# Kernel tuning notes

Hardware: AMD Instinct MI355X
Metric: run time of the kernel (lower is better)

The kernel has to match this reference:

```python
import jax, jax.numpy as jnp
import numpy as np

N = 50000          # nodes
E = 800000         # edges (before self-loops)
IN_CH = 16
HID = 32
HEADS = 4
NEG_SLOPE = 0.2    # PyG GATConv default leaky_relu slope


def add_self_loops(edge_index, n):
    loops = jnp.arange(n, dtype=edge_index.dtype)
    return jnp.concatenate([edge_index, jnp.stack([loops, loops])], axis=1)


def gat_layer(x, edge_index, W, a_src, a_dst, bias, heads, out_ch, concat):
    """PyG-style GATConv: gather -> attention logits -> segment softmax over dst -> scatter."""
    n = x.shape[0]
    h = (x @ W).reshape(n, heads, out_ch)            # [N, H, C]
    src, dst = edge_index[0], edge_index[1]          # messages flow src -> dst
    alpha_src = (h * a_src).sum(-1)                  # [N, H]
    alpha_dst = (h * a_dst).sum(-1)                  # [N, H]
    e = jax.nn.leaky_relu(alpha_src[src] + alpha_dst[dst], NEG_SLOPE)  # [Etot, H]
    # numerically stable segment softmax over incoming edges of each dst node
    e_max = jax.ops.segment_max(e, dst, num_segments=n)
    e_exp = jnp.exp(e - e_max[dst])
    denom = jax.ops.segment_sum(e_exp, dst, num_segments=n)
    alpha = e_exp / (denom[dst] + 1e-16)             # [Etot, H]
    out = jax.ops.segment_sum(h[src] * alpha[..., None], dst, num_segments=n)  # [N, H, C]
    out = out.reshape(n, heads * out_ch) if concat else out.mean(axis=1)
    return out + bias


def setup_inputs() -> dict:
    key = jax.random.key(0)
    ks = jax.random.split(key, 10)
    x = jax.random.normal(ks[0], (N, IN_CH), dtype=jnp.float32)
    edge_index = jax.random.randint(ks[1], (2, E), 0, N, dtype=jnp.int64)
    s = 0.1
    W1 = jax.random.normal(ks[2], (IN_CH, HEADS * HID), dtype=jnp.float32) * s
    a_src1 = jax.random.normal(ks[3], (1, HEADS, HID), dtype=jnp.float32) * s
    a_dst1 = jax.random.normal(ks[4], (1, HEADS, HID), dtype=jnp.float32) * s
    b1 = jnp.zeros((HEADS * HID,), dtype=jnp.float32)
    W2 = jax.random.normal(ks[5], (HEADS * HID, 2), dtype=jnp.float32) * s
    a_src2 = jax.random.normal(ks[6], (1, 1, 2), dtype=jnp.float32) * s
    a_dst2 = jax.random.normal(ks[7], (1, 1, 2), dtype=jnp.float32) * s
    b2 = jnp.zeros((2,), dtype=jnp.float32)
    return {"x": x, "edge_index": edge_index,
            "W1": W1, "a_src1": a_src1, "a_dst1": a_dst1, "b1": b1,
            "W2": W2, "a_src2": a_src2, "a_dst2": a_dst2, "b2": b2}


def reference(x, edge_index, W1, a_src1, a_dst1, b1, W2, a_src2, a_dst2, b2):
    ei = add_self_loops(edge_index, x.shape[0])
    h = gat_layer(x, ei, W1, a_src1, a_dst1, b1, HEADS, HID, concat=True)
    h = jax.nn.relu(h)
    out = gat_layer(h, ei, W2, a_src2, a_dst2, b2, 1, 2, concat=False)
    return out
```

## Files before the change

kernel.cpp:

```cpp
#include <hip/hip_runtime.h>
#include <hip/hip_bf16.h>

#define N_NODES 50000
#define N_EDGES 800000
#define ETOT    (N_EDGES + N_NODES)
#define STRIDE  64
#define IN_CH   16
#define HID     32
#define HEADS   4
#define C1      (HEADS * HID)
#define NEG     0.2f

#define DEG_BLOCKS ((ETOT / 4 + 255) / 256)
#define NGROUPS    (N_NODES / 4)
#define H1_BLOCKS  2048

typedef unsigned short u16;
typedef unsigned int   u32;

__device__ __forceinline__ float bf2f(u16 b) {
    return __uint_as_float(((u32)b) << 16);
}

__device__ __forceinline__ u16 f2bf(float f) {
    __hip_bfloat16 hb = __float2bfloat16(f);
    return *(u16*)&hb;
}

__device__ __forceinline__ int clampn(int v) {
    return v < 0 ? 0 : (v >= N_NODES ? N_NODES - 1 : v);
}

__device__ __forceinline__ int eidx(const int* ei, int e, int i64, int which) {
    int v = i64 ? ei[2 * (which * N_EDGES + e)] : ei[which * N_EDGES + e];
    return clampn(v);
}

__device__ __forceinline__ float cvt(const void* src, int i, int bf) {
    return bf ? bf2f(((const u16*)src)[i]) : ((const float*)src)[i];
}

__device__ __forceinline__ int probe_bf_wave(const u16* xb) {
    int l = threadIdx.x & 63;
    int my = 0;
#pragma unroll
    for (int k = 0; k < 4; k++) {
        float f = bf2f(xb[l * 4 + k]);
        float a = fabsf(f);
        if (f == 0.0f || (a > 9.5e-7f && a < 1.05e6f)) my++;
    }
#pragma unroll
    for (int m = 32; m; m >>= 1) my += __shfl_xor(my, m);
    return my >= 224;
}

__device__ __forceinline__ int probe_i64_wave(const int* ei32) {
    int l = threadIdx.x & 63;
    int nz = (l < 32 && ei32[2 * l + 1] != 0) ? 1 : 0;
#pragma unroll
    for (int m = 32; m; m >>= 1) nz += __shfl_xor(nz, m);
    return nz == 0;
}

__device__ __forceinline__ void dev_deg(const int* __restrict__ ei,
                                        int* __restrict__ degs,
                                        u32* __restrict__ srp, int blk) {
    int i64 = probe_i64_wave(ei);
    int e0 = (blk * 256 + (int)threadIdx.x) * 4;
    if (e0 >= ETOT) return;
    int s[4], d[4];
#pragma unroll
    for (int j = 0; j < 4; j++) {
        int e = e0 + j;
        if (e < N_EDGES) { s[j] = eidx(ei, e, i64, 0); d[j] = eidx(ei, e, i64, 1); }
        else             { s[j] = d[j] = e - N_EDGES; }
    }
    u32 r[4];
#pragma unroll
    for (int j = 0; j < 4; j++) {
        u32 rr = (u32)atomicAdd(&degs[d[j]], 1);
        r[j] = ((u32)s[j] << 16) | (rr > 0xFFFFu ? 0xFFFFu : rr);
    }
    *(uint4*)(srp + e0) = make_uint4(r[0], r[1], r[2], r[3]);
}

__device__ __forceinline__ void dev_fill(const int* __restrict__ ei,
                                         const u32* __restrict__ srp,
                                         u16* __restrict__ csr, int blk) {
    int i64 = probe_i64_wave(ei);
    int e0 = (blk * 256 + (int)threadIdx.x) * 4;
    if (e0 >= ETOT) return;
    uint4 q = *(const uint4*)(srp + e0);
    u32 sr[4] = {q.x, q.y, q.z, q.w};
#pragma unroll
    for (int j = 0; j < 4; j++) {
        int e = e0 + j;
        int d = (e < N_EDGES) ? eidx(ei, e, i64, 1) : (e - N_EDGES);
        u32 r = sr[j] & 0xFFFFu;
        if (r < STRIDE) csr[d * STRIDE + r] = (u16)(sr[j] >> 16);
    }
}

__device__ __forceinline__ void dev_h1(const void* __restrict__ x,
                                       const void* __restrict__ W1,
                                       const void* __restrict__ a_s,
                                       const void* __restrict__ a_d,
                                       u32* __restrict__ h1u,
                                       float* __restrict__ as1,
                                       float* __restrict__ ad1,
                                       float* Ws, float* As, float* Ad, int blk) {
    int bf = probe_bf_wave((const u16*)x);
    if (blk == 0 && threadIdx.x < 4) as1[N_NODES * 4 + threadIdx.x] = -1e30f;
    if (bf) {
        const u32* w32 = (const u32*)W1;
        for (int i = threadIdx.x; i < IN_CH * C1 / 2; i += 256) {
            u32 v = w32[i];
            Ws[2 * i]     = bf2f((u16)(v & 0xFFFF));
            Ws[2 * i + 1] = bf2f((u16)(v >> 16));
        }
        const u32* s32 = (const u32*)a_s;
        const u32* d32 = (const u32*)a_d;
        for (int i = threadIdx.x; i < C1 / 2; i += 256) {
            u32 vs = s32[i], vd = d32[i];
            As[2 * i]     = bf2f((u16)(vs & 0xFFFF));
            As[2 * i + 1] = bf2f((u16)(vs >> 16));
            Ad[2 * i]     = bf2f((u16)(vd & 0xFFFF));
            Ad[2 * i + 1] = bf2f((u16)(vd >> 16));
        }
    } else {
        for (int i = threadIdx.x; i < IN_CH * C1; i += 256) Ws[i] = ((const float*)W1)[i];
        for (int i = threadIdx.x; i < C1; i += 256) {
            As[i] = ((const float*)a_s)[i];
            Ad[i] = ((const float*)a_d)[i];
        }
    }
    __syncthreads();

    int w = threadIdx.x >> 6, l = threadIdx.x & 63;
    int c0 = 2 * l, c1 = 2 * l + 1;
    for (int g = blk; g < NGROUPS; g += H1_BLOCKS) {
        int n = g * 4 + w;
        float xval = (l < IN_CH) ? cvt(x, n * IN_CH + l, bf) : 0.f;
        float acc0 = 0.f, acc1 = 0.f;
#pragma unroll
        for (int k = 0; k < IN_CH; k++) {
            float xk = __shfl(xval, k);
            acc0 += xk * Ws[k * C1 + c0];
            acc1 += xk * Ws[k * C1 + c1];
        }
        h1u[n * 64 + l] = (u32)f2bf(acc0) | ((u32)f2bf(acc1) << 16);

        float ps = acc0 * As[c0] + acc1 * As[c1];
        float pd = acc0 * Ad[c0] + acc1 * Ad[c1];
#pragma unroll
        for (int m = 8; m; m >>= 1) { ps += __shfl_xor(ps, m); pd += __shfl_xor(pd, m); }
        if ((l & 15) == 0) {
            int hd = l >> 4;
            as1[n * 4 + hd] = ps;
            ad1[n * 4 + hd] = pd;
        }
    }
}

__launch_bounds__(256)
__global__ void k_deg(const int* __restrict__ ei, int* __restrict__ degs,
                      u32* __restrict__ srp) {
    dev_deg(ei, degs, srp, blockIdx.x);
}

__launch_bounds__(256)
__global__ void k_fill_h1(const void* __restrict__ x, const int* __restrict__ ei,
                          const void* __restrict__ W1, const void* __restrict__ a_s,
                          const void* __restrict__ a_d, const u32* __restrict__ srp,
                          u16* __restrict__ csr, u32* __restrict__ h1u,
                          float* __restrict__ as1, float* __restrict__ ad1) {
    __shared__ float Ws[IN_CH * C1];
    __shared__ float As[C1], Ad[C1];
    if (blockIdx.x < DEG_BLOCKS) { dev_fill(ei, srp, csr, blockIdx.x); return; }
    dev_h1(x, W1, a_s, a_d, h1u, as1, ad1, Ws, As, Ad, blockIdx.x - DEG_BLOCKS);
}

__launch_bounds__(256)
__global__ void k_fill(const int* __restrict__ ei, const u32* __restrict__ srp,
                       u16* __restrict__ csr) {
    dev_fill(ei, srp, csr, blockIdx.x);
}

__launch_bounds__(256)
__global__ void k_h1_only(const void* __restrict__ x, const void* __restrict__ W1,
                          const void* __restrict__ a_s, const void* __restrict__ a_d,
                          u32* __restrict__ h1u, float* __restrict__ as1,
                          float* __restrict__ ad1) {
    __shared__ float Ws[IN_CH * C1];
    __shared__ float As[C1], Ad[C1];
    dev_h1(x, W1, a_s, a_d, h1u, as1, ad1, Ws, As, Ad, blockIdx.x);
}

__launch_bounds__(256)
__global__ void k_gather1(const void* __restrict__ x,
                          const int* __restrict__ degs, const u16* __restrict__ csr,
                          const u32* __restrict__ h1u,
                          const float* __restrict__ as1, const float* __restrict__ ad1,
                          const void* __restrict__ b1, const void* __restrict__ W2,
                          const void* __restrict__ a2s, const void* __restrict__ a2d,
                          float* __restrict__ h2, float* __restrict__ as2,
                          float* __restrict__ ad2) {
    int bf = probe_bf_wave((const u16*)x);
    int n = blockIdx.x * 4 + (threadIdx.x >> 6);
    int l = threadIdx.x & 63;
    int hd = l >> 4;
    int jb = l & 15;
    float adv = ad1[n * 4 + hd];
    int deg = degs[n]; deg = deg > STRIDE ? STRIDE : deg;
    int nb = (deg + 15) >> 4;
    const u16* row = csr + (size_t)n * STRIDE;
    float acc0 = 0.f, acc1 = 0.f, sw = 0.f;

    for (int b = 0; b < nb; b++) {
        int se = (int)row[b * 16 + jb];
        if (se >= N_NODES) se = N_NODES;
        float t = as1[se * 4 + hd] + adv;
        t = t > 0.f ? t : NEG * t;
        float wm = __expf(t);
#pragma unroll
        for (int j = 0; j < 16; j++) {
            int   sj = __shfl(se, j);
            float wj = __shfl(wm, hd * 16 + j);
            u32 p = h1u[sj * 64 + l];
            sw   += wj;
            acc0 += wj * bf2f((u16)(p & 0xFFFF));
            acc1 += wj * bf2f((u16)(p >> 16));
        }
    }

    float inv = 1.0f / sw;
    float v0 = acc0 * inv + cvt(b1, 2 * l, bf);
    float v1 = acc1 * inv + cvt(b1, 2 * l + 1, bf);
    v0 = v0 > 0.f ? v0 : 0.f;
    v1 = v1 > 0.f ? v1 : 0.f;
    float p0 = v0 * cvt(W2, 4 * l,     bf) + v1 * cvt(W2, 4 * l + 2, bf);
    float p1 = v0 * cvt(W2, 4 * l + 1, bf) + v1 * cvt(W2, 4 * l + 3, bf);
#pragma unroll
    for (int d = 32; d; d >>= 1) { p0 += __shfl_down(p0, d); p1 += __shfl_down(p1, d); }
    if (l == 0) {
        h2[n * 2] = p0; h2[n * 2 + 1] = p1;
        as2[n] = p0 * cvt(a2s, 0, bf) + p1 * cvt(a2s, 1, bf);
        ad2[n] = p0 * cvt(a2d, 0, bf) + p1 * cvt(a2d, 1, bf);
    }
}

__launch_bounds__(256)
__global__ void k_gather2(const void* __restrict__ x,
                          const int* __restrict__ degs, const u16* __restrict__ csr,
                          const float* __restrict__ h2, const float* __restrict__ as2,
                          const float* __restrict__ ad2, const void* __restrict__ b2,
                          void* __restrict__ out) {
    int bf = probe_bf_wave((const u16*)x);
    int n = blockIdx.x * 16 + (threadIdx.x >> 4);
    int g = threadIdx.x & 15;
    float adv = ad2[n], a0 = 0.f, a1 = 0.f, sw = 0.f;
    int deg = degs[n]; deg = deg > STRIDE ? STRIDE : deg;
    const u16* row = csr + (size_t)n * STRIDE;
    for (int k = g; k < deg; k += 16) {
        int s = (int)row[k];
        float lg = as2[s] + adv;
        lg = lg > 0.f ? lg : NEG * lg;
        float w = __expf(lg);
        float2 hv = ((const float2*)h2)[s];
        a0 += w * hv.x;
        a1 += w * hv.y;
        sw += w;
    }
#pragma unroll
    for (int m = 8; m; m >>= 1) {
        a0 += __shfl_xor(a0, m); a1 += __shfl_xor(a1, m); sw += __shfl_xor(sw, m);
    }
    if (g == 0) {
        float inv = 1.0f / sw;
        float o0 = a0 * inv + cvt(b2, 0, bf);
        float o1 = a1 * inv + cvt(b2, 1, bf);
        if (bf) {
            ((u32*)out)[n] = (u32)f2bf(o0) | ((u32)f2bf(o1) << 16);
        } else {
            ((float2*)out)[n] = make_float2(o0, o1);
        }
    }
}

extern "C" void kernel_launch(void* const* d_in, const int* in_sizes, int n_in,
                              void* d_out, int out_size, void* d_ws, size_t ws_size,
                              hipStream_t stream) {
    const void* x    = d_in[0];
    const int*  ei   = (const int*)d_in[1];
    const void* W1   = d_in[2];
    const void* a_s1 = d_in[3];
    const void* a_d1 = d_in[4];
    const void* b1   = d_in[5];
    const void* W2   = d_in[6];
    const void* a_s2 = d_in[7];
    const void* a_d2 = d_in[8];
    const void* b2   = d_in[9];

    char* p = (char*)d_ws;
    int*   degs = (int*)p;     p += ((size_t)N_NODES * 4 + 255) & ~255;
    u16*   csr  = (u16*)p;     p += (size_t)N_NODES * STRIDE * 2;
    u32*   h1u  = (u32*)p;     p += (size_t)(N_NODES + 1) * 64 * 4;
    float* as1  = (float*)p;   p += (size_t)(N_NODES + 1) * HEADS * 4;
    float* ad1  = (float*)p;   p += (size_t)N_NODES * HEADS * 4;
    float* h2   = (float*)p;   p += (size_t)N_NODES * 2 * 4;
    float* as2  = (float*)p;   p += (size_t)N_NODES * 4;
    float* ad2  = (float*)p;   p += (size_t)N_NODES * 4;
    size_t base_used = (size_t)(p - (char*)d_ws);
    size_t srp_bytes = (size_t)ETOT * 4;

    hipMemsetAsync(degs, 0, (size_t)N_NODES * sizeof(int), stream);
    hipMemsetAsync(csr, 0xFF, (size_t)N_NODES * STRIDE * 2, stream);

    if (ws_size >= base_used + srp_bytes) {
        u32* srp = (u32*)p;
        k_deg<<<DEG_BLOCKS, 256, 0, stream>>>(ei, degs, srp);
        k_fill_h1<<<DEG_BLOCKS + H1_BLOCKS, 256, 0, stream>>>(
            x, ei, W1, a_s1, a_d1, srp, csr, h1u, as1, ad1);
    } else {
        u32* srp = h1u;
        k_deg<<<DEG_BLOCKS, 256, 0, stream>>>(ei, degs, srp);
        k_fill<<<DEG_BLOCKS, 256, 0, stream>>>(ei, srp, csr);
        k_h1_only<<<H1_BLOCKS, 256, 0, stream>>>(x, W1, a_s1, a_d1, h1u, as1, ad1);
    }
    k_gather1<<<N_NODES / 4, 256, 0, stream>>>(
        x, degs, csr, h1u, as1, ad1, b1, W2, a_s2, a_d2, h2, as2, ad2);
    k_gather2<<<N_NODES / 16, 256, 0, stream>>>(
        x, degs, csr, h2, as2, ad2, b2, d_out);
}
```

Measured before the change: 208.8 us.

## Process two nodes per wave in layer-1 gather with 8-byte row loads

The layer-1 aggregation kernel now packs two destination nodes into each 64-lane wave. Each half-wave handles one node, loads 4 bf16 features per lane as a uint2, and processes edges in chunks of 8 instead of 16. The goal is fewer wasted lanes on low-degree nodes (the average in-degree is about 17) and wider memory transactions per gathered row. The two halves loop to the larger of their two chunk counts, so padding chunks (index clamped to N_NODES) add some extra work when degrees differ. The final reduction is now a 32-lane xor shuffle.

Result: slower. 216.0 us (+3.4%).

```diff
diff --git a/kernel.cpp b/kernel.cpp
--- a/kernel.cpp
+++ b/kernel.cpp
@@ -206,43 +206,58 @@
                           float* __restrict__ h2, float* __restrict__ as2,
                           float* __restrict__ ad2) {
     int bf = probe_bf_wave((const u16*)x);
-    int n = blockIdx.x * 4 + (threadIdx.x >> 6);
-    int l = threadIdx.x & 63;
-    int hd = l >> 4;
-    int jb = l & 15;
+    int l    = threadIdx.x & 63;
+    int kk   = l & 31;
+    int base = l & 32;
+    int wv   = threadIdx.x >> 6;
+    int n    = blockIdx.x * 8 + wv * 2 + (l >> 5);
+    int hd   = kk >> 3;
+    int je   = kk & 7;
     float adv = ad1[n * 4 + hd];
     int deg = degs[n]; deg = deg > STRIDE ? STRIDE : deg;
-    int nb = (deg + 15) >> 4;
+    int nb = (deg + 7) >> 3;
+    int onb = __shfl_xor(nb, 32);
+    int nbmax = nb > onb ? nb : onb;
     const u16* row = csr + (size_t)n * STRIDE;
-    float acc0 = 0.f, acc1 = 0.f, sw = 0.f;
-
-    for (int b = 0; b < nb; b++) {
-        int se = (int)row[b * 16 + jb];
+    float acc0 = 0.f, acc1 = 0.f, acc2 = 0.f, acc3 = 0.f, sw = 0.f;
+
+    for (int b = 0; b < nbmax; b++) {
+        int se = (int)row[b * 8 + je];
         if (se >= N_NODES) se = N_NODES;
         float t = as1[se * 4 + hd] + adv;
         t = t > 0.f ? t : NEG * t;
         float wm = __expf(t);
 #pragma unroll
-        for (int j = 0; j < 16; j++) {
-            int   sj = __shfl(se, j);
-            float wj = __shfl(wm, hd * 16 + j);
-            u32 p = h1u[sj * 64 + l];
+        for (int j = 0; j < 8; j++) {
+            int   sj = __shfl(se, base + j);
+            float wj = __shfl(wm, base + hd * 8 + j);
+            uint2 pp = *(const uint2*)(h1u + (size_t)sj * 64 + 2 * kk);
             sw   += wj;
-            acc0 += wj * bf2f((u16)(p & 0xFFFF));
-            acc1 += wj * bf2f((u16)(p >> 16));
+            acc0 += wj * bf2f((u16)(pp.x & 0xFFFF));
+            acc1 += wj * bf2f((u16)(pp.x >> 16));
+            acc2 += wj * bf2f((u16)(pp.y & 0xFFFF));
+            acc3 += wj * bf2f((u16)(pp.y >> 16));
         }
     }
 
     float inv = 1.0f / sw;
-    float v0 = acc0 * inv + cvt(b1, 2 * l, bf);
-    float v1 = acc1 * inv + cvt(b1, 2 * l + 1, bf);
-    v0 = v0 > 0.f ? v0 : 0.f;
-    v1 = v1 > 0.f ? v1 : 0.f;
-    float p0 = v0 * cvt(W2, 4 * l,     bf) + v1 * cvt(W2, 4 * l + 2, bf);
-    float p1 = v0 * cvt(W2, 4 * l + 1, bf) + v1 * cvt(W2, 4 * l + 3, bf);
-#pragma unroll
-    for (int d = 32; d; d >>= 1) { p0 += __shfl_down(p0, d); p1 += __shfl_down(p1, d); }
-    if (l == 0) {
+    int c = 4 * kk;
+    float v0 = acc0 * inv + cvt(b1, c,     bf);
+    float v1 = acc1 * inv + cvt(b1, c + 1, bf);
+    float v2 = acc2 * inv + cvt(b1, c + 2, bf);
+    float v3 = acc3 * inv + cvt(b1, c + 3, bf);
+    v0 = v0 > 0.f ? v0 : 0.f;  v1 = v1 > 0.f ? v1 : 0.f;
+    v2 = v2 > 0.f ? v2 : 0.f;  v3 = v3 > 0.f ? v3 : 0.f;
+    float p0 = v0 * cvt(W2, 2 * c,     bf) + v1 * cvt(W2, 2 * c + 2, bf)
+             + v2 * cvt(W2, 2 * c + 4, bf) + v3 * cvt(W2, 2 * c + 6, bf);
+    float p1 = v0 * cvt(W2, 2 * c + 1, bf) + v1 * cvt(W2, 2 * c + 3, bf)
+             + v2 * cvt(W2, 2 * c + 5, bf) + v3 * cvt(W2, 2 * c + 7, bf);
+#pragma unroll
+    for (int m = 16; m; m >>= 1) {
+        p0 += __shfl_xor(p0, m);
+        p1 += __shfl_xor(p1, m);
+    }
+    if (kk == 0) {
         h2[n * 2] = p0; h2[n * 2 + 1] = p1;
         as2[n] = p0 * cvt(a2s, 0, bf) + p1 * cvt(a2s, 1, bf);
         ad2[n] = p0 * cvt(a2d, 0, bf) + p1 * cvt(a2d, 1, bf);
@@ -327,7 +342,7 @@
         k_fill<<<DEG_BLOCKS, 256, 0, stream>>>(ei, srp, csr);
         k_h1_only<<<H1_BLOCKS, 256, 0, stream>>>(x, W1, a_s1, a_d1, h1u, as1, ad1);
     }
-    k_gather1<<<N_NODES / 4, 256, 0, stream>>>(
+    k_gather1<<<N_NODES / 8, 256, 0, stream>>>(
         x, degs, csr, h1u, as1, ad1, b1, W2, a_s2, a_d2, h2, as2, ad2);
     k_gather2<<<N_NODES / 16, 256, 0, stream>>>(
         x, degs, csr, h2, as2, ad2, b2, d_out);
```
